# Kernel optimization log

Hardware: AMD Instinct MI355X
Metric: run time of the kernel (lower is better)

## Reference

```python
import jax, jax.numpy as jnp
import numpy as np

# Static sizes (RED-GNN on ICEWS14-like graph)
B = 32          # batch (queries)
N = 100000      # active nodes per layer (fixed frontier size)
E = 1000000     # edges per layer
H = 64          # hidden_dim
A = 5           # attn_dim
L = 3           # n_layer
N_REL = 230
N_ENT = 7128
N_TIME = 365


def setup_inputs() -> dict:
    key = jax.random.key(0)
    ks = jax.random.split(key, 16)
    inp = {}
    # edge structure (constant w.r.t. differentiation)
    inp['batch_idx'] = jax.random.randint(ks[0], (E,), 0, B)
    inp['src_idx'] = jax.random.randint(ks[1], (E,), 0, N)
    inp['dst_idx'] = jax.random.randint(ks[2], (E,), 0, N)
    inp['rel_idx'] = jax.random.randint(ks[3], (E,), 0, N_REL + 1)
    # signed relative time in [-(N_TIME-1), N_TIME-1]
    inp['rel_time'] = jax.random.randint(ks[4], (E,), -(N_TIME - 1), N_TIME)
    inp['query_rel'] = jax.random.randint(ks[5], (B,), 0, N_REL + 1)
    # unique (batch, entity) slot per final node
    n = jnp.arange(N)
    inp['out_batch'] = n // N_ENT
    inp['out_ent'] = n % N_ENT
    # learned parameters
    s = 1.0 / np.sqrt(H)
    inp['rela_embed'] = jax.random.normal(ks[6], (L, N_REL + 1, H), jnp.float32) * s
    inp['time_embed'] = jax.random.normal(ks[7], (N_TIME, H), jnp.float32) * s
    inp['Wp'] = jax.random.normal(ks[8], (H, H), jnp.float32) * s
    inp['Wn'] = jax.random.normal(ks[9], (H, H), jnp.float32) * s
    inp['Wf'] = jax.random.normal(ks[10], (H, H), jnp.float32) * s
    inp['W1'] = jax.random.normal(ks[11], (L, A, 3 * H), jnp.float32) * s
    inp['W2'] = jax.random.normal(ks[12], (L, 1, A), jnp.float32) / np.sqrt(A)
    inp['Wc'] = jax.random.normal(ks[13], (1, H), jnp.float32) * s
    inp['bc'] = jnp.zeros((1,), jnp.float32)
    return inp


def reference(rela_embed, time_embed, Wp, Wn, Wf, W1, W2, Wc, bc,
              batch_idx, src_idx, dst_idx, rel_idx, rel_time,
              query_rel, out_batch, out_ent):
    hidden = jnp.zeros((N, H), dtype=rela_embed.dtype)
    q_rel_e = query_rel[batch_idx]                 # [E]
    t_emb = time_embed[jnp.abs(rel_time)]          # [E,H]
    pos = (rel_time > 0)[:, None]
    zer = (rel_time == 0)[:, None]
    for i in range(L):
        rel_e = rela_embed[i][rel_idx]             # [E,H]
        embed = hidden[src_idx] + rel_e + t_emb    # [E,H]
        # branch by sign of relative time: future / now / past linear
        transformed = jnp.where(pos, embed @ Wf.T,
                      jnp.where(zer, embed @ Wn.T, embed @ Wp.T))
        attn_in = jnp.concatenate(
            [hidden[src_idx], rel_e, rela_embed[i][q_rel_e]], axis=1)  # [E,3H]
        score = jax.nn.sigmoid(
            jax.nn.relu(attn_in @ W1[i].T) @ W2[i].T)  # [E,1]
        msg = score * transformed                      # [E,H]
        hidden = jax.nn.relu(
            jax.ops.segment_sum(msg, dst_idx, num_segments=N))
    result = (hidden @ Wc.T + bc).reshape(-1)          # [N]
    score_all = jnp.zeros((B, N_ENT), result.dtype)
    score_all = score_all.at[out_batch, out_ent].set(result)
    return score_all
```

## Files before the change

### kernel.cpp

```cpp
#include <hip/hip_runtime.h>

#define NB   32
#define NN   100000
#define NE   1000000
#define HD   64
#define AD   5
#define NL   3
#define NRL  231
#define NTM  365
#define NOUT 228096
#define NBLK1 391


__device__ __forceinline__ float bflo(unsigned u) { return __uint_as_float(u << 16); }
__device__ __forceinline__ float bfhi(unsigned u) { return __uint_as_float(u & 0xffff0000u); }
__device__ __forceinline__ unsigned packbf2(float x, float y) {
    unsigned ux = __float_as_uint(x), uy = __float_as_uint(y);
    ux = (ux + 0x7fffu + ((ux >> 16) & 1u)) >> 16;
    uy = (uy + 0x7fffu + ((uy >> 16) & 1u)) >> 16;
    return ux | (uy << 16);
}

__global__ __launch_bounds__(256) void prep_wt_kernel(
    const float* __restrict__ Wp, const float* __restrict__ Wn,
    const float* __restrict__ Wf, float* __restrict__ WT)
{
    int i = blockIdx.x * 256 + threadIdx.x;
    if (i >= 3 * 64 * 64) return;
    int c = i >> 12;
    int k = (i >> 6) & 63;
    int h = i & 63;
    const float* W = (c == 0) ? Wf : (c == 1 ? Wn : Wp);
    WT[i] = W[h * 64 + k];
}

__global__ __launch_bounds__(256) void prep_tables_kernel(
    const float* __restrict__ rela_embed,
    const float* __restrict__ W1,
    float* __restrict__ Trel,
    float* __restrict__ Tq)
{
    int l = blockIdx.x;
    int r = threadIdx.x;
    if (r >= NRL) return;
    const float4* rrow = (const float4*)(rela_embed + ((size_t)l * NRL + r) * HD);
    const float* W1l = W1 + (size_t)l * AD * 192;
    float tr[AD] = {0,0,0,0,0}, tq[AD] = {0,0,0,0,0};
    #pragma unroll
    for (int k4 = 0; k4 < 16; ++k4) {
        float4 x = rrow[k4];
        #pragma unroll
        for (int a = 0; a < AD; ++a) {
            const float* wr = W1l + a * 192 + 64 + k4 * 4;
            const float* wq = W1l + a * 192 + 128 + k4 * 4;
            tr[a] = fmaf(x.x, wr[0], tr[a]); tr[a] = fmaf(x.y, wr[1], tr[a]);
            tr[a] = fmaf(x.z, wr[2], tr[a]); tr[a] = fmaf(x.w, wr[3], tr[a]);
            tq[a] = fmaf(x.x, wq[0], tq[a]); tq[a] = fmaf(x.y, wq[1], tq[a]);
            tq[a] = fmaf(x.z, wq[2], tq[a]); tq[a] = fmaf(x.w, wq[3], tq[a]);
        }
    }
    float* tro = Trel + ((size_t)l * NRL + r) * 8;
    float* tqo = Tq   + ((size_t)l * NRL + r) * 8;
    #pragma unroll
    for (int a = 0; a < AD; ++a) { tro[a] = tr[a]; tqo[a] = tq[a]; }
    tro[5] = tro[6] = tro[7] = 0.f;
    tqo[5] = tqo[6] = tqo[7] = 0.f;
}

__global__ __launch_bounds__(256) void hist_kernel(
    const int* __restrict__ dst_idx, int* __restrict__ deg)
{
    int e = blockIdx.x * 256 + threadIdx.x;
    if (e < NE) atomicAdd(&deg[dst_idx[e]], 1);
}

__global__ __launch_bounds__(256) void scan1_kernel(
    const int* __restrict__ deg, int* __restrict__ tmp, int* __restrict__ bsum)
{
    __shared__ int s[256];
    int tid = threadIdx.x;
    int i = blockIdx.x * 256 + tid;
    int v = (i < NN) ? deg[i] : 0;
    s[tid] = v;
    __syncthreads();
    #pragma unroll
    for (int st = 1; st < 256; st <<= 1) {
        int t = (tid >= st) ? s[tid - st] : 0;
        __syncthreads();
        s[tid] += t;
        __syncthreads();
    }
    if (i < NN) tmp[i] = s[tid];
    if (tid == 255) bsum[blockIdx.x] = s[255];
}

__global__ __launch_bounds__(512) void scan2_kernel(
    const int* __restrict__ bsum, int* __restrict__ bpref)
{
    __shared__ int s[512];
    int tid = threadIdx.x;
    int v = (tid < NBLK1) ? bsum[tid] : 0;
    s[tid] = v;
    __syncthreads();
    #pragma unroll
    for (int st = 1; st < 512; st <<= 1) {
        int t = (tid >= st) ? s[tid - st] : 0;
        __syncthreads();
        s[tid] += t;
        __syncthreads();
    }
    if (tid < NBLK1) bpref[tid] = s[tid] - v;
}

__global__ __launch_bounds__(256) void scan3_kernel(
    const int* __restrict__ deg, const int* __restrict__ tmp,
    const int* __restrict__ bpref, int* __restrict__ off, int* __restrict__ cursor)
{
    int i = blockIdx.x * 256 + threadIdx.x;
    if (i >= NN) return;
    int incl = tmp[i] + bpref[i >> 8];
    off[i + 1] = incl;
    cursor[i] = incl - deg[i];
    if (i == 0) off[0] = 0;
}

__global__ __launch_bounds__(256) void sort_scatter_kernel(
    const int* __restrict__ dst_idx, const int* __restrict__ src_idx,
    const int* __restrict__ rel_idx, const int* __restrict__ rel_time,
    const int* __restrict__ batch_idx, const int* __restrict__ query_rel,
    const float* __restrict__ Trel0, const float* __restrict__ Tq0,
    const float* __restrict__ W2,
    int* __restrict__ cursor, int2* __restrict__ meta,
    float* __restrict__ score0)
{
    int e = blockIdx.x * 256 + threadIdx.x;
    if (e >= NE) return;
    int d = dst_idx[e];
    int rt = rel_time[e];
    int cls = (rt > 0) ? 0 : ((rt == 0) ? 1 : 2);
    int ta = (rt < 0) ? -rt : rt;
    int rel = rel_idx[e];
    int q = query_rel[batch_idx[e]];
    int pos = atomicAdd(&cursor[d], 1);
    int2 m;
    m.x = src_idx[e] | (rel << 17) | (cls << 25);
    m.y = ta | (q << 9);
    meta[pos] = m;

    float4 t0 = *(const float4*)(Trel0 + rel * 8);
    float  t4 = Trel0[rel * 8 + 4];
    float4 u0 = *(const float4*)(Tq0 + q * 8);
    float  u4 = Tq0[q * 8 + 4];
    float z = 0.f;
    z = fmaf(fmaxf(t0.x + u0.x, 0.f), W2[0], z);
    z = fmaf(fmaxf(t0.y + u0.y, 0.f), W2[1], z);
    z = fmaf(fmaxf(t0.z + u0.z, 0.f), W2[2], z);
    z = fmaf(fmaxf(t0.w + u0.w, 0.f), W2[3], z);
    z = fmaf(fmaxf(t4   + u4,   0.f), W2[4], z);
    score0[pos] = 1.f / (1.f + __expf(-z));
}

__global__ __launch_bounds__(256) void score_kernel(
    const float* __restrict__ proj,
    const float* __restrict__ Trel,
    const float* __restrict__ Tq,
    const float* __restrict__ W2,
    const int2* __restrict__ meta,
    float* __restrict__ score)
{
    int j = blockIdx.x * 256 + threadIdx.x;
    if (j >= NE) return;
    int2 mt = meta[j];
    int rel = (mt.x >> 17) & 0xFF;
    int q   = (mt.y >> 9) & 0xFF;
    int src = mt.x & 0x1FFFF;

    float4 t0 = *(const float4*)(Trel + rel * 8);
    float  t4 = Trel[rel * 8 + 4];
    float4 u0 = *(const float4*)(Tq + q * 8);
    float  u4 = Tq[q * 8 + 4];
    float4 p0 = *(const float4*)(proj + (size_t)src * 8);
    float  p4 = proj[(size_t)src * 8 + 4];
    float z = 0.f;
    z = fmaf(fmaxf(p0.x + t0.x + u0.x, 0.f), W2[0], z);
    z = fmaf(fmaxf(p0.y + t0.y + u0.y, 0.f), W2[1], z);
    z = fmaf(fmaxf(p0.z + t0.z + u0.z, 0.f), W2[2], z);
    z = fmaf(fmaxf(p0.w + t0.w + u0.w, 0.f), W2[3], z);
    z = fmaf(fmaxf(p4   + t4   + u4,   0.f), W2[4], z);
    score[j] = 1.f / (1.f + __expf(-z));
}

template <bool HZ>
__device__ __forceinline__ void edge1(
    int2 m, float sc, int hc8,
    const ushort* __restrict__ hidden_in,
    const float* __restrict__ rela, const float* __restrict__ temb,
    float4* __restrict__ A)
{
    int src = m.x & 0x1FFFF, rel = (m.x >> 17) & 0xFF;
    int cl  = (m.x >> 25) & 3, ta = m.y & 511;
    const float* rp = rela + rel * HD + hc8;
    const float* tp = temb + ta * HD + hc8;
    float4 rv0 = *(const float4*)rp;
    float4 rv1 = *(const float4*)(rp + 4);
    float4 tv0 = *(const float4*)tp;
    float4 tv1 = *(const float4*)(tp + 4);
    float4 v0, v1;
    v0.x = rv0.x + tv0.x; v0.y = rv0.y + tv0.y;
    v0.z = rv0.z + tv0.z; v0.w = rv0.w + tv0.w;
    v1.x = rv1.x + tv1.x; v1.y = rv1.y + tv1.y;
    v1.z = rv1.z + tv1.z; v1.w = rv1.w + tv1.w;
    if (!HZ) {
        uint4 hv = *(const uint4*)(hidden_in + (size_t)src * HD + hc8);
        v0.x += bflo(hv.x); v0.y += bfhi(hv.x);
        v0.z += bflo(hv.y); v0.w += bfhi(hv.y);
        v1.x += bflo(hv.z); v1.y += bfhi(hv.z);
        v1.z += bflo(hv.w); v1.w += bfhi(hv.w);
    }
    float sA = (cl == 0) ? sc : 0.f;
    float sB = (cl == 1) ? sc : 0.f;
    float sC = (cl == 2) ? sc : 0.f;
    A[0].x = fmaf(sA, v0.x, A[0].x); A[0].y = fmaf(sA, v0.y, A[0].y);
    A[0].z = fmaf(sA, v0.z, A[0].z); A[0].w = fmaf(sA, v0.w, A[0].w);
    A[1].x = fmaf(sA, v1.x, A[1].x); A[1].y = fmaf(sA, v1.y, A[1].y);
    A[1].z = fmaf(sA, v1.z, A[1].z); A[1].w = fmaf(sA, v1.w, A[1].w);
    A[2].x = fmaf(sB, v0.x, A[2].x); A[2].y = fmaf(sB, v0.y, A[2].y);
    A[2].z = fmaf(sB, v0.z, A[2].z); A[2].w = fmaf(sB, v0.w, A[2].w);
    A[3].x = fmaf(sB, v1.x, A[3].x); A[3].y = fmaf(sB, v1.y, A[3].y);
    A[3].z = fmaf(sB, v1.z, A[3].z); A[3].w = fmaf(sB, v1.w, A[3].w);
    A[4].x = fmaf(sC, v0.x, A[4].x); A[4].y = fmaf(sC, v0.y, A[4].y);
    A[4].z = fmaf(sC, v0.z, A[4].z); A[4].w = fmaf(sC, v0.w, A[4].w);
    A[5].x = fmaf(sC, v1.x, A[5].x); A[5].y = fmaf(sC, v1.y, A[5].y);
    A[5].z = fmaf(sC, v1.z, A[5].z); A[5].w = fmaf(sC, v1.w, A[5].w);
}

#define LPITCH 65
template <bool HZ, bool PROJ>
__global__ __launch_bounds__(256, 4) void reduce_transform_kernel(
    const ushort* __restrict__ hidden_in,
    const float* __restrict__ rela,
    const float* __restrict__ temb,
    const float* __restrict__ score,
    const int2* __restrict__ meta,
    const int*  __restrict__ off,
    const float* __restrict__ WT,
    const float* __restrict__ W1next,
    ushort* __restrict__ hidden_out,
    float* __restrict__ proj_out)
{
    __shared__ float lds_t[64 * LPITCH];
    int tid  = threadIdx.x;
    int lane = tid & 63;
    int w    = __builtin_amdgcn_readfirstlane(tid >> 6);
    int g    = lane >> 3;
    int hc   = lane & 7;
    int hc8  = hc * 8;
    int node0 = blockIdx.x * 64;
    int h0 = w * 16;

    float4 a[2][6];
    #pragma unroll
    for (int rr = 0; rr < 2; ++rr)
        #pragma unroll
        for (int c = 0; c < 6; ++c)
            a[rr][c] = make_float4(0.f, 0.f, 0.f, 0.f);

    #pragma unroll
    for (int rr = 0; rr < 2; ++rr) {
        int nl = w * 16 + rr * 8 + g;
        int node = node0 + nl;
        if (node >= NN) continue;
        int o0 = off[node];
        int o1 = off[node + 1];
        int j = o0;
        for (; j + 2 <= o1; j += 2) {
            int2 m0 = meta[j], m1 = meta[j + 1];
            float s0 = score[j], s1 = score[j + 1];
            edge1<HZ>(m0, s0, hc8, hidden_in, rela, temb, a[rr]);
            edge1<HZ>(m1, s1, hc8, hidden_in, rela, temb, a[rr]);
        }
        if (j < o1)
            edge1<HZ>(meta[j], score[j], hc8, hidden_in, rela, temb, a[rr]);
    }

    float acc[16];
    #pragma unroll
    for (int i = 0; i < 16; ++i) acc[i] = 0.f;

    #pragma unroll
    for (int c = 0; c < 3; ++c) {
        __syncthreads();
        #pragma unroll
        for (int rr = 0; rr < 2; ++rr) {
            int nl = w * 16 + rr * 8 + g;
            float4 lo = a[rr][2 * c];
            float4 hi = a[rr][2 * c + 1];
            lds_t[(hc8 + 0) * LPITCH + nl] = lo.x;
            lds_t[(hc8 + 1) * LPITCH + nl] = lo.y;
            lds_t[(hc8 + 2) * LPITCH + nl] = lo.z;
            lds_t[(hc8 + 3) * LPITCH + nl] = lo.w;
            lds_t[(hc8 + 4) * LPITCH + nl] = hi.x;
            lds_t[(hc8 + 5) * LPITCH + nl] = hi.y;
            lds_t[(hc8 + 6) * LPITCH + nl] = hi.z;
            lds_t[(hc8 + 7) * LPITCH + nl] = hi.w;
        }
        __syncthreads();
        const float* __restrict__ Wb = WT + (c * 64) * 64 + h0;
        #pragma unroll 4
        for (int k = 0; k < 64; ++k) {
            float av = lds_t[k * LPITCH + lane];
            #pragma unroll
            for (int i = 0; i < 16; ++i)
                acc[i] = fmaf(av, Wb[k * 64 + i], acc[i]);
        }
    }

    int node = node0 + lane;
    if (node < NN) {
        ushort* outp = hidden_out + (size_t)node * 64 + h0;
        unsigned up[8];
        #pragma unroll
        for (int p = 0; p < 8; ++p)
            up[p] = packbf2(fmaxf(acc[2 * p], 0.f), fmaxf(acc[2 * p + 1], 0.f));
        *(uint4*)(outp)     = make_uint4(up[0], up[1], up[2], up[3]);
        *(uint4*)(outp + 8) = make_uint4(up[4], up[5], up[6], up[7]);
    }

    if (PROJ) {
        float pa[AD];
        #pragma unroll
        for (int aa = 0; aa < AD; ++aa) pa[aa] = 0.f;
        #pragma unroll
        for (int i = 0; i < 16; ++i) {
            float hv = fmaxf(acc[i], 0.f);
            #pragma unroll
            for (int aa = 0; aa < AD; ++aa)
                pa[aa] = fmaf(hv, W1next[aa * 192 + h0 + i], pa[aa]);
        }
        __syncthreads();
        float* lds2 = lds_t;
        #pragma unroll
        for (int aa = 0; aa < AD; ++aa)
            lds2[(w * 64 + lane) * AD + aa] = pa[aa];
        __syncthreads();
        for (int idx = tid; idx < 64 * 8; idx += 256) {
            int nd = idx >> 3, aa = idx & 7;
            if (node0 + nd >= NN) break;
            float v = 0.f;
            if (aa < AD) {
                #pragma unroll
                for (int w4 = 0; w4 < 4; ++w4)
                    v += lds2[(w4 * 64 + nd) * AD + aa];
            }
            proj_out[(size_t)(node0 + nd) * 8 + aa] = v;
        }
    }
}

__global__ __launch_bounds__(256) void out_kernel(
    const ushort* __restrict__ hidden,
    const float* __restrict__ Wc,
    const float* __restrict__ bc,
    float* __restrict__ out)
{
    int i = blockIdx.x * 256 + threadIdx.x;
    if (i >= NOUT) return;
    float r = 0.f;
    if (i < NN) {
        const uint4* h4 = (const uint4*)(hidden + (size_t)i * 64);
        float acc = 0.f;
        #pragma unroll
        for (int q = 0; q < 8; ++q) {
            uint4 hv = h4[q];
            const float* wq = Wc + q * 8;
            acc = fmaf(bflo(hv.x), wq[0], acc);
            acc = fmaf(bfhi(hv.x), wq[1], acc);
            acc = fmaf(bflo(hv.y), wq[2], acc);
            acc = fmaf(bfhi(hv.y), wq[3], acc);
            acc = fmaf(bflo(hv.z), wq[4], acc);
            acc = fmaf(bfhi(hv.z), wq[5], acc);
            acc = fmaf(bflo(hv.w), wq[6], acc);
            acc = fmaf(bfhi(hv.w), wq[7], acc);
        }
        r = acc + bc[0];
    }
    out[i] = r;
}

extern "C" void kernel_launch(void* const* d_in, const int* in_sizes, int n_in,
                              void* d_out, int out_size, void* d_ws, size_t ws_size,
                              hipStream_t stream)
{
    const int*   batch_idx  = (const int*)d_in[0];
    const int*   src_idx    = (const int*)d_in[1];
    const int*   dst_idx    = (const int*)d_in[2];
    const int*   rel_idx    = (const int*)d_in[3];
    const int*   rel_time   = (const int*)d_in[4];
    const int*   query_rel  = (const int*)d_in[5];
    const float* rela_embed = (const float*)d_in[8];
    const float* time_embed = (const float*)d_in[9];
    const float* Wp         = (const float*)d_in[10];
    const float* Wn         = (const float*)d_in[11];
    const float* Wf         = (const float*)d_in[12];
    const float* W1         = (const float*)d_in[13];
    const float* W2         = (const float*)d_in[14];
    const float* Wc         = (const float*)d_in[15];
    const float* bc         = (const float*)d_in[16];
    float* out = (float*)d_out;

    char* ws = (char*)d_ws;
    ushort* hid0  = (ushort*)(ws + 0);
    ushort* hid1  = (ushort*)(ws + 12800000);
    float* projA  = (float*)(ws + 25600000);
    float* projB  = (float*)(ws + 28800000);
    float* score  = (float*)(ws + 32000000);
    float* WT     = (float*)(ws + 36000000);
    float* Trel   = (float*)(ws + 36100000);
    float* Tq     = (float*)(ws + 36130000);
    int*   off    = (int*)  (ws + 36160000);
    int2*  meta   = (int2*) (ws + 37400000);
    int*   deg    = (int*)  (ws + 45400000);
    int*   tmp    = (int*)  (ws + 46600000);
    int*   cursor = (int*)  (ws + 47800000);
    int*   bsum   = (int*)  (ws + 49000000);
    int*   bpref  = (int*)  (ws + 49010000);

    prep_wt_kernel<<<48, 256, 0, stream>>>(Wp, Wn, Wf, WT);
    prep_tables_kernel<<<NL, 256, 0, stream>>>(rela_embed, W1, Trel, Tq);

    hipMemsetAsync(deg, 0, NN * sizeof(int), stream);
    hist_kernel<<<(NE + 255) / 256, 256, 0, stream>>>(dst_idx, deg);
    scan1_kernel<<<NBLK1, 256, 0, stream>>>(deg, tmp, bsum);
    scan2_kernel<<<1, 512, 0, stream>>>(bsum, bpref);
    scan3_kernel<<<NBLK1, 256, 0, stream>>>(deg, tmp, bpref, off, cursor);
    sort_scatter_kernel<<<(NE + 255) / 256, 256, 0, stream>>>(
        dst_idx, src_idx, rel_idx, rel_time, batch_idx, query_rel,
        Trel, Tq, W2, cursor, meta, score);

    int grid = (NN + 63) / 64;
    int sgrid = (NE + 255) / 256;
    {
        reduce_transform_kernel<true, true><<<grid, 256, 0, stream>>>(
            hid1, rela_embed, time_embed, score, meta, off,
            WT, W1 + (size_t)1 * AD * 192, hid0, projA);
    }
    {
        const float* rela = rela_embed + (size_t)1 * NRL * HD;
        score_kernel<<<sgrid, 256, 0, stream>>>(
            projA, Trel + (size_t)1 * NRL * 8, Tq + (size_t)1 * NRL * 8,
            W2 + 1 * AD, meta, score);
        reduce_transform_kernel<false, true><<<grid, 256, 0, stream>>>(
            hid0, rela, time_embed, score, meta, off,
            WT, W1 + (size_t)2 * AD * 192, hid1, projB);
    }
    {
        const float* rela = rela_embed + (size_t)2 * NRL * HD;
        score_kernel<<<sgrid, 256, 0, stream>>>(
            projB, Trel + (size_t)2 * NRL * 8, Tq + (size_t)2 * NRL * 8,
            W2 + 2 * AD, meta, score);
        reduce_transform_kernel<false, false><<<grid, 256, 0, stream>>>(
            hid1, rela, time_embed, score, meta, off,
            WT, nullptr, hid0, nullptr);
    }

    out_kernel<<<(NOUT + 255) / 256, 256, 0, stream>>>(hid0, Wc, bc, out);
}
```

Measured before the change: 465.2 us.

## Replace scalar FMA transform GEMM with split-bf16 MFMA in reduce kernel

```diff
diff --git a/kernel.cpp b/kernel.cpp
--- a/kernel.cpp
+++ b/kernel.cpp
@@ -21,17 +21,37 @@
     return ux | (uy << 16);
 }
 
-__global__ __launch_bounds__(256) void prep_wt_kernel(
+using vbf8  = __attribute__((ext_vector_type(8))) short;
+using f32x4 = __attribute__((ext_vector_type(4))) float;
+
+__global__ __launch_bounds__(256) void prep_wtb_kernel(
     const float* __restrict__ Wp, const float* __restrict__ Wn,
-    const float* __restrict__ Wf, float* __restrict__ WT)
+    const float* __restrict__ Wf, ushort* __restrict__ WTB)
 {
     int i = blockIdx.x * 256 + threadIdx.x;
-    if (i >= 3 * 64 * 64) return;
-    int c = i >> 12;
-    int k = (i >> 6) & 63;
-    int h = i & 63;
+    if (i >= 3072) return;
+    int lane = i & 63;
+    int nt = (i >> 6) & 3;
+    int ks = (i >> 8) & 1;
+    int hl = (i >> 9) & 1;
+    int c  = i >> 10;
     const float* W = (c == 0) ? Wf : (c == 1 ? Wn : Wp);
-    WT[i] = W[h * 64 + k];
+    int h  = nt * 16 + (lane & 15);
+    int k0 = ks * 32 + (lane >> 4) * 8;
+    unsigned up[4];
+    #pragma unroll
+    for (int j = 0; j < 4; ++j) {
+        float x = W[h * 64 + k0 + 2 * j];
+        float y = W[h * 64 + k0 + 2 * j + 1];
+        unsigned pb = packbf2(x, y);
+        if (hl) {
+            float rx = x - bflo(pb);
+            float ry = y - bfhi(pb);
+            pb = packbf2(rx, ry);
+        }
+        up[j] = pb;
+    }
+    *(uint4*)(WTB + (size_t)i * 8) = make_uint4(up[0], up[1], up[2], up[3]);
 }
 
 __global__ __launch_bounds__(256) void prep_tables_kernel(
@@ -234,7 +254,7 @@
     A[5].z = fmaf(sC, v1.z, A[5].z); A[5].w = fmaf(sC, v1.w, A[5].w);
 }
 
-#define LPITCH 65
+#define SPITCH 68
 template <bool HZ, bool PROJ>
 __global__ __launch_bounds__(256, 4) void reduce_transform_kernel(
     const ushort* __restrict__ hidden_in,
@@ -243,12 +263,12 @@
     const float* __restrict__ score,
     const int2* __restrict__ meta,
     const int*  __restrict__ off,
-    const float* __restrict__ WT,
+    const ushort* __restrict__ WTB,
     const float* __restrict__ W1next,
     ushort* __restrict__ hidden_out,
     float* __restrict__ proj_out)
 {
-    __shared__ float lds_t[64 * LPITCH];
+    __shared__ float lds_t[64 * SPITCH];
     int tid  = threadIdx.x;
     int lane = tid & 63;
     int w    = __builtin_amdgcn_readfirstlane(tid >> 6);
@@ -283,9 +303,13 @@
             edge1<HZ>(meta[j], score[j], hc8, hidden_in, rela, temb, a[rr]);
     }
 
-    float acc[16];
-    #pragma unroll
-    for (int i = 0; i < 16; ++i) acc[i] = 0.f;
+    unsigned* lds_u = (unsigned*)lds_t;
+    int rl = lane & 15;
+    int t  = lane >> 4;
+    f32x4 accd[4];
+    #pragma unroll
+    for (int nt = 0; nt < 4; ++nt)
+        accd[nt] = (f32x4){0.f, 0.f, 0.f, 0.f};
 
     #pragma unroll
     for (int c = 0; c < 3; ++c) {
@@ -293,25 +317,54 @@
         #pragma unroll
         for (int rr = 0; rr < 2; ++rr) {
             int nl = w * 16 + rr * 8 + g;
-            float4 lo = a[rr][2 * c];
-            float4 hi = a[rr][2 * c + 1];
-            lds_t[(hc8 + 0) * LPITCH + nl] = lo.x;
-            lds_t[(hc8 + 1) * LPITCH + nl] = lo.y;
-            lds_t[(hc8 + 2) * LPITCH + nl] = lo.z;
-            lds_t[(hc8 + 3) * LPITCH + nl] = lo.w;
-            lds_t[(hc8 + 4) * LPITCH + nl] = hi.x;
-            lds_t[(hc8 + 5) * LPITCH + nl] = hi.y;
-            lds_t[(hc8 + 6) * LPITCH + nl] = hi.z;
-            lds_t[(hc8 + 7) * LPITCH + nl] = hi.w;
-        }
-        __syncthreads();
-        const float* __restrict__ Wb = WT + (c * 64) * 64 + h0;
-        #pragma unroll 4
-        for (int k = 0; k < 64; ++k) {
-            float av = lds_t[k * LPITCH + lane];
+            float4 v0 = a[rr][2 * c];
+            float4 v1 = a[rr][2 * c + 1];
+            unsigned p0 = packbf2(v0.x, v0.y);
+            unsigned p1 = packbf2(v0.z, v0.w);
+            unsigned p2 = packbf2(v1.x, v1.y);
+            unsigned p3 = packbf2(v1.z, v1.w);
+            unsigned q0 = packbf2(v0.x - bflo(p0), v0.y - bfhi(p0));
+            unsigned q1 = packbf2(v0.z - bflo(p1), v0.w - bfhi(p1));
+            unsigned q2 = packbf2(v1.x - bflo(p2), v1.y - bfhi(p2));
+            unsigned q3 = packbf2(v1.z - bflo(p3), v1.w - bfhi(p3));
+            *(uint4*)(lds_u + nl * SPITCH + hc * 4)      = make_uint4(p0, p1, p2, p3);
+            *(uint4*)(lds_u + nl * SPITCH + 32 + hc * 4) = make_uint4(q0, q1, q2, q3);
+        }
+        __syncthreads();
+        #pragma unroll
+        for (int ks = 0; ks < 2; ++ks) {
+            const unsigned* rowp = lds_u + (w * 16 + rl) * SPITCH + ks * 16 + t * 4;
+            vbf8 ah = *(const vbf8*)rowp;
+            vbf8 al = *(const vbf8*)(rowp + 32);
             #pragma unroll
-            for (int i = 0; i < 16; ++i)
-                acc[i] = fmaf(av, Wb[k * 64 + i], acc[i]);
+            for (int nt = 0; nt < 4; ++nt) {
+                const ushort* bp = WTB +
+                    (size_t)((((c * 2) * 2 + ks) * 4 + nt) * 64 + lane) * 8;
+                vbf8 bh = *(const vbf8*)bp;
+                vbf8 bl = *(const vbf8*)(bp + 4096);
+                accd[nt] = __builtin_amdgcn_mfma_f32_16x16x32_bf16(ah, bh, accd[nt], 0, 0, 0);
+                accd[nt] = __builtin_amdgcn_mfma_f32_16x16x32_bf16(al, bh, accd[nt], 0, 0, 0);
+                accd[nt] = __builtin_amdgcn_mfma_f32_16x16x32_bf16(ah, bl, accd[nt], 0, 0, 0);
+            }
+        }
+    }
+
+    __syncthreads();
+    #pragma unroll
+    for (int nt = 0; nt < 4; ++nt)
+        #pragma unroll
+        for (int i = 0; i < 4; ++i)
+            lds_t[(w * 16 + t * 4 + i) * SPITCH + nt * 16 + rl] = accd[nt][i];
+    __syncthreads();
+
+    float acc[16];
+    {
+        const float4* rp = (const float4*)(lds_t + lane * SPITCH + h0);
+        #pragma unroll
+        for (int i4 = 0; i4 < 4; ++i4) {
+            float4 v = rp[i4];
+            acc[i4 * 4 + 0] = v.x; acc[i4 * 4 + 1] = v.y;
+            acc[i4 * 4 + 2] = v.z; acc[i4 * 4 + 3] = v.w;
         }
     }
 
@@ -414,7 +467,7 @@
     float* projA  = (float*)(ws + 25600000);
     float* projB  = (float*)(ws + 28800000);
     float* score  = (float*)(ws + 32000000);
-    float* WT     = (float*)(ws + 36000000);
+    ushort* WTB   = (ushort*)(ws + 36000000);
     float* Trel   = (float*)(ws + 36100000);
     float* Tq     = (float*)(ws + 36130000);
     int*   off    = (int*)  (ws + 36160000);
@@ -425,7 +478,7 @@
     int*   bsum   = (int*)  (ws + 49000000);
     int*   bpref  = (int*)  (ws + 49010000);
 
-    prep_wt_kernel<<<48, 256, 0, stream>>>(Wp, Wn, Wf, WT);
+    prep_wtb_kernel<<<12, 256, 0, stream>>>(Wp, Wn, Wf, WTB);
     prep_tables_kernel<<<NL, 256, 0, stream>>>(rela_embed, W1, Trel, Tq);
 
     hipMemsetAsync(deg, 0, NN * sizeof(int), stream);
@@ -442,7 +495,7 @@
     {
         reduce_transform_kernel<true, true><<<grid, 256, 0, stream>>>(
             hid1, rela_embed, time_embed, score, meta, off,
-            WT, W1 + (size_t)1 * AD * 192, hid0, projA);
+            WTB, W1 + (size_t)1 * AD * 192, hid0, projA);
     }
     {
         const float* rela = rela_embed + (size_t)1 * NRL * HD;
@@ -451,7 +504,7 @@
             W2 + 1 * AD, meta, score);
         reduce_transform_kernel<false, true><<<grid, 256, 0, stream>>>(
             hid0, rela, time_embed, score, meta, off,
-            WT, W1 + (size_t)2 * AD * 192, hid1, projB);
+            WTB, W1 + (size_t)2 * AD * 192, hid1, projB);
     }
     {
         const float* rela = rela_embed + (size_t)2 * NRL * HD;
@@ -460,7 +513,7 @@
             W2 + 2 * AD, meta, score);
         reduce_transform_kernel<false, false><<<grid, 256, 0, stream>>>(
             hid1, rela, time_embed, score, meta, off,
-            WT, nullptr, hid0, nullptr);
+            WTB, nullptr, hid0, nullptr);
     }
 
     out_kernel<<<(NOUT + 255) / 256, 256, 0, stream>>>(hid0, Wc, bc, out);
```

Result: faster. 424.8 us (-8.7%).
